# Kernel optimization log

Measured on AMD Instinct MI355X. Metric: run time of the kernel, lower is better.

The kernel has to match this reference:

```python
import jax, jax.numpy as jnp
import numpy as np

# Explicit-duration HSMM forward DP in log space.
# Recursion (all quantities in log space):
#   entry[t, j] = pi[j]                                   if t == 0
#               = logsumexp_i alpha[t-1, i] + A[i, j]      otherwise
#   alpha[t, j] = logsumexp_{d=1..min(Dmax, t+1)}
#                   entry[t-d+1, j] + D[j, d] + sum_{u=t-d+1..t} log_B[u, j]
#   loglik      = logsumexp_j alpha[T-1, j]

NEG = -1.0e30  # finite -inf sentinel (autodiff-safe)
B, T, S, DMAX = 64, 2048, 128, 128


def setup_inputs() -> dict:
    key = jax.random.key(0)
    k1, k2, k3, k4 = jax.random.split(key, 4)
    # emission log-likelihoods per (batch, time, state); need not normalize over states
    log_B = jax.random.normal(k1, (B, T, S), dtype=jnp.float32)
    # normalized log-prob buffers, matching the module's buffer constraints
    pi_logits = jax.nn.log_softmax(jax.random.normal(k2, (S,), dtype=jnp.float32))
    A_raw = jax.random.normal(k3, (S, S), dtype=jnp.float32)
    # SEMI transition constraint: no self-transitions (diagonal ~ -inf), rows normalized
    A_logits = jax.nn.log_softmax(
        jnp.where(jnp.eye(S, dtype=bool), -1.0e9, A_raw), axis=1)
    D_logits = jax.nn.log_softmax(
        jax.random.normal(k4, (S, DMAX), dtype=jnp.float32), axis=1)
    return {"log_B": log_B, "pi_logits": pi_logits,
            "A_logits": A_logits, "D_logits": D_logits}


def _hsmm_forward_loglik(log_B, pi_logits, A_logits, D_logits):
    Bn, Tn, Sn = log_B.shape
    Dm = D_logits.shape[1]
    lb = jnp.transpose(log_B, (1, 0, 2))                         # (T, B, S)
    # cum[k] = sum_{u < k} log_B[u]; front-padded with Dm zero rows (masked anyway)
    cum = jnp.concatenate(
        [jnp.zeros((1, Bn, Sn), lb.dtype), jnp.cumsum(lb, axis=0)], axis=0)
    cum_pad = jnp.concatenate(
        [jnp.zeros((Dm, Bn, Sn), lb.dtype), cum], axis=0)        # (T+Dm+1, B, S)
    logD = D_logits.T[:, None, :]                                # (Dm, 1, S)
    dur = jnp.arange(1, Dm + 1)[:, None, None]                   # (Dm, 1, 1)

    def step(carry, t):
        entry_buf, alpha_prev = carry                            # (Dm,B,S), (B,S)
        # transition into state j after a segment ended at t-1
        trans = jax.nn.logsumexp(
            alpha_prev[:, :, None] + A_logits[None, :, :], axis=1)  # (B, S)
        entry_t = jnp.where(t == 0, pi_logits[None, :], trans)
        # entry_buf[d-1] = entry[t-d+1]
        entry_buf = jnp.roll(entry_buf, 1, axis=0).at[0].set(entry_t)
        # segment emission sums: seg[d-1] = cum[t+1] - cum[t+1-d]
        win = jax.lax.dynamic_slice_in_dim(cum_pad, t + 1, Dm, axis=0)
        end = jax.lax.dynamic_slice_in_dim(cum_pad, t + Dm + 1, 1, axis=0)
        seg = end - jnp.flip(win, axis=0)                        # (Dm, B, S)
        scores = entry_buf + logD + seg
        scores = jnp.where(dur <= t + 1, scores, NEG)            # mask d > t+1
        alpha_t = jax.nn.logsumexp(scores, axis=0)               # (B, S)
        return (entry_buf, alpha_t), None

    init = (jnp.full((Dm, Bn, Sn), NEG, lb.dtype),
            jnp.full((Bn, Sn), NEG, lb.dtype))
    (_, alpha_last), _ = jax.lax.scan(step, init, jnp.arange(Tn))
    return jax.nn.logsumexp(alpha_last, axis=1)                  # (B,)


def reference(log_B, pi_logits, A_logits, D_logits):
    return _hsmm_forward_loglik(log_B, pi_logits, A_logits, D_logits)
```

## Files before the change

kernel.cpp:

```cpp
#include <hip/hip_runtime.h>

#define TT 2048
#define SS 128
#define DMAXX 128
#define NBATCH 64

typedef float f2 __attribute__((ext_vector_type(2)));

__device__ __forceinline__ float fexp2(float x){ return __builtin_amdgcn_exp2f(x); }
__device__ __forceinline__ float flog2(float x){ return __builtin_amdgcn_logf(x); }
__device__ __forceinline__ float frcp (float x){ return __builtin_amdgcn_rcpf(x); }
__device__ __forceinline__ f2 pkfma(f2 a, f2 b, f2 c){ return __builtin_elementwise_fma(a, b, c); }

template<int CTRL>
__device__ __forceinline__ float dppf(float x) {
    int i = __float_as_int(x);
    return __int_as_float(__builtin_amdgcn_update_dpp(i, i, CTRL, 0xF, 0xF, false));
}
template<int CTRL>
__device__ __forceinline__ float dppzf(float x) {
    int i = __float_as_int(x);
    return __int_as_float(__builtin_amdgcn_update_dpp(0, i, CTRL, 0xF, 0xF, true));
}
#define DPP_XOR1   0xB1
#define DPP_XOR2   0x4E
#define DPP_RSHR4  0x114
#define DPP_ROR4   0x124
#define DPP_ROR8   0x128
#define DPP_BC15   0x142
#define DPP_BC31   0x143

constexpr float LOG2E = 1.4426950408889634f;
constexpr float LN2   = 0.6931471805599453f;

struct State {
    f2    rp[16];
    f2    eApk[16];
    f2    eDp[32];
    float eD0;
    float pf[4];
    const float* pfp;
    float C2;
    float e_pi;
    float G;
    float dsP;
};

struct Ctx {
    const float4* up0; const float4* up1;
    const f2*     wmp;
    float* uaw0; float* uaw1;
    float* wmwp;
    bool q0, l63, b0, b1;
};

template<int P>
__device__ __forceinline__ void hsmm_step(State& st, const Ctx& c, int tb8)
{
    constexpr int  rho    = 31 - P;
    constexpr int  rhoN   = 30 - P;
    constexpr int  pb     = (P + 1) & 1;
    constexpr int  wb     = P & 1;
    constexpr bool DO_WM  = (P == 6);
    constexpr bool DO_RN  = (P == 7);
    constexpr bool REBASE = (P == 7);
    const int t = tb8 + P;

    const float4* up = pb ? c.up1 : c.up0;
    float4 va = up[0];
    float4 vb = up[1];

    float xB = st.pf[P & 3];
    if (t + 4 < TT) st.pf[P & 3] = st.pfp[P * SS];
    if constexpr (P == 7) st.pfp += 8 * SS;

    float g = fexp2(xB * LOG2E);
    if constexpr (DO_RN) {
        f2 wv = *c.wmp;
        float m = fmaxf(wv.x, wv.y);
        m = fmaxf(m, dppf<DPP_XOR1>(m));
        m = fmaxf(m, dppf<DPP_XOR2>(m));
        st.C2 += flog2(m);
        g *= frcp(m);
    }
    float rG = frcp(st.G);
    float Gn = st.G * g;
    st.G = Gn;

    f2 a0, a1, a2, a3, u;
    u = (f2){va.x, va.y};
    a0 = u * st.eApk[0];  a1 = u * st.eApk[4];  a2 = u * st.eApk[8];  a3 = u * st.eApk[12];
    u = (f2){va.z, va.w};
    a0 = pkfma(u, st.eApk[1], a0); a1 = pkfma(u, st.eApk[5], a1);
    a2 = pkfma(u, st.eApk[9], a2); a3 = pkfma(u, st.eApk[13], a3);
    u = (f2){vb.x, vb.y};
    a0 = pkfma(u, st.eApk[2], a0); a1 = pkfma(u, st.eApk[6], a1);
    a2 = pkfma(u, st.eApk[10], a2); a3 = pkfma(u, st.eApk[14], a3);
    u = (f2){vb.z, vb.w};
    a0 = pkfma(u, st.eApk[3], a0); a1 = pkfma(u, st.eApk[7], a1);
    a2 = pkfma(u, st.eApk[11], a2); a3 = pkfma(u, st.eApk[15], a3);

    float h0 = a0.x + a0.y, h1 = a1.x + a1.y, h2 = a2.x + a2.y, h3 = a3.x + a3.y;
    float s1 = c.b0 ? h0 : h1;
    float k1 = c.b0 ? h1 : h0;
    float m01 = k1 + dppf<DPP_XOR1>(s1);
    float s2 = c.b0 ? h2 : h3;
    float k2 = c.b0 ? h3 : h2;
    float m23 = k2 + dppf<DPP_XOR1>(s2);
    float s3 = c.b1 ? m01 : m23;
    float k3 = c.b1 ? m23 : m01;
    float tp = k3 + dppf<DPP_XOR2>(s3);
    tp += dppf<DPP_ROR4>(tp);
    tp += dppf<DPP_ROR8>(tp);
    if constexpr (P == 0) { if (tb8 == 0) tp = st.e_pi; }

    float U = fmaf(tp * g, st.eD0, st.dsP * Gn);
    if (c.q0) {
        float fr = tp * rG;
        if constexpr (rho & 1) st.rp[rho >> 1].y = fr;
        else                   st.rp[rho >> 1].x = fr;
        *(wb ? c.uaw1 : c.uaw0) = U;
    }

    if constexpr (DO_WM) {
        float wm = U;
        wm = fmaxf(wm, dppf<DPP_XOR1>(wm));
        wm = fmaxf(wm, dppf<DPP_XOR2>(wm));
        wm = fmaxf(wm, dppf<DPP_BC15>(wm));
        wm = fmaxf(wm, dppf<DPP_BC31>(wm));
        if (c.l63) *c.wmwp = wm;
    }

    if constexpr (REBASE) {
        f2 GG = {Gn, Gn};
#pragma unroll
        for (int m2 = 0; m2 < 16; ++m2) st.rp[m2] = st.rp[m2] * GG;
        st.G = 1.f;
    }

    float rold;
    if constexpr (rhoN & 1) rold = st.rp[rhoN >> 1].y; else rold = st.rp[rhoN >> 1].x;
    float ins = dppzf<DPP_RSHR4>(rold);
    if constexpr (rhoN & 1) st.rp[rhoN >> 1].y = ins;
    else                    st.rp[rhoN >> 1].x = ins;

    f2 q0a = {0.f, 0.f}, q1a = {0.f, 0.f}, q2a = {0.f, 0.f}, q3a = {0.f, 0.f};
#pragma unroll
    for (int m2 = 0; m2 < 16; m2 += 4) {
        q0a = pkfma(st.rp[m2],     st.eDp[(2 * m2 + P + 2) & 31], q0a);
        q1a = pkfma(st.rp[m2 + 1], st.eDp[(2 * m2 + P + 4) & 31], q1a);
        q2a = pkfma(st.rp[m2 + 2], st.eDp[(2 * m2 + P + 6) & 31], q2a);
        q3a = pkfma(st.rp[m2 + 3], st.eDp[(2 * m2 + P + 8) & 31], q3a);
    }
    f2 qs = (q0a + q1a) + (q2a + q3a);
    float ds = qs.x + qs.y;
    ds += dppf<DPP_ROR4>(ds);
    ds += dppf<DPP_ROR8>(ds);
    st.dsP = ds;

    asm volatile("s_waitcnt lgkmcnt(0)\n\ts_barrier" ::: "memory");
}

__launch_bounds__(512, 2)
__global__ void hsmm_fwd_kernel(const float* __restrict__ logB,
                                const float* __restrict__ pi,
                                const float* __restrict__ A,
                                const float* __restrict__ D,
                                float* __restrict__ out)
{
    const int b    = blockIdx.x;
    const int tid  = threadIdx.x;
    const int l    = tid & 63;
    const int w    = tid >> 6;
    const int r    = (l >> 4);
    const int sIdx = l & 15;
    const int cc   = l & 3;
    const int q    = (l >> 2) & 3;
    const int j4   = w * 16 + r * 4;
    const int j    = j4 + cc;

    __shared__ __align__(16) float ua[2][16 * 12];
    __shared__ __align__(16) float wmaxf[8];

    State st;
#pragma unroll
    for (int cp = 0; cp < 4; ++cp)
#pragma unroll
        for (int m = 0; m < 4; ++m) {
            st.eApk[cp * 4 + m].x = fexp2(A[(8 * sIdx + 2 * m)     * SS + j4 + cp] * LOG2E);
            st.eApk[cp * 4 + m].y = fexp2(A[(8 * sIdx + 2 * m + 1) * SS + j4 + cp] * LOG2E);
        }
    {
        float eD[32];
#pragma unroll
        for (int k = 0; k < 32; ++k)
            eD[k] = fexp2(D[j * DMAXX + q * 32 + k] * LOG2E);
#pragma unroll
        for (int wdx = 0; wdx < 32; ++wdx) {
            st.eDp[wdx].x = eD[wdx];
            st.eDp[wdx].y = eD[(wdx + 1) & 31];
        }
    }
#pragma unroll
    for (int k = 0; k < 16; ++k) st.rp[k] = (f2){0.f, 0.f};
    st.eD0  = fexp2(D[j * DMAXX] * LOG2E);
    st.C2   = 0.f;
    st.e_pi = fexp2(pi[j] * LOG2E);
    st.G    = 1.f;
    st.dsP  = 0.f;

    const float* __restrict__ lb = logB + ((size_t)b * TT) * SS + j;
#pragma unroll
    for (int k = 0; k < 4; ++k) st.pf[k] = lb[(size_t)k * SS];
    st.pfp = lb + (size_t)4 * SS;

    Ctx c;
    c.up0  = (const float4*)&ua[0][sIdx * 12];
    c.up1  = (const float4*)&ua[1][sIdx * 12];
    c.wmp  = (const f2*)&wmaxf[2 * cc];
    c.q0   = (q == 0);
    c.l63  = (l == 63);
    c.b0   = (l & 1);
    c.b1   = ((l & 2) != 0);
    c.uaw0 = &ua[0][(j >> 3) * 12 + (j & 7)];
    c.uaw1 = &ua[1][(j >> 3) * 12 + (j & 7)];
    c.wmwp = &wmaxf[w];

#pragma unroll 1
    for (int tb8 = 0; tb8 < TT; tb8 += 8) {
        hsmm_step<0>(st, c, tb8); hsmm_step<1>(st, c, tb8);
        hsmm_step<2>(st, c, tb8); hsmm_step<3>(st, c, tb8);
        hsmm_step<4>(st, c, tb8); hsmm_step<5>(st, c, tb8);
        hsmm_step<6>(st, c, tb8); hsmm_step<7>(st, c, tb8);
        {
            f2 t12 = st.rp[12], t13 = st.rp[13], t14 = st.rp[14], t15 = st.rp[15];
            st.rp[15] = st.rp[11]; st.rp[14] = st.rp[10];
            st.rp[13] = st.rp[9];  st.rp[12] = st.rp[8];
            st.rp[11] = st.rp[7];  st.rp[10] = st.rp[6];
            st.rp[9]  = st.rp[5];  st.rp[8]  = st.rp[4];
            st.rp[7]  = st.rp[3];  st.rp[6]  = st.rp[2];
            st.rp[5]  = st.rp[1];  st.rp[4]  = st.rp[0];
            st.rp[3] = t15; st.rp[2] = t14; st.rp[1] = t13; st.rp[0] = t12;
        }
    }

    if (tid == 0) {
        float s = 0.f;
        for (int i = 0; i < SS; ++i) s += ua[1][(i >> 3) * 12 + (i & 7)];
        out[b] = (st.C2 + flog2(s)) * LN2;
    }
}

extern "C" void kernel_launch(void* const* d_in, const int* in_sizes, int n_in,
                              void* d_out, int out_size, void* d_ws, size_t ws_size,
                              hipStream_t stream) {
    const float* logB = (const float*)d_in[0];
    const float* pi   = (const float*)d_in[1];
    const float* A    = (const float*)d_in[2];
    const float* D    = (const float*)d_in[3];
    float* out        = (float*)d_out;
    hipLaunchKernelGGL(hsmm_fwd_kernel, dim3(NBATCH), dim3(512), 0, stream,
                       logB, pi, A, D, out);
}
```

Measured before the change: 825.6 us.

## Halve block to 256 threads with each lane owning two states

The block shrinks from 8 waves to 4, and each thread now carries two state roles (j and j+64), each with its own A, D and ring registers. The per-step barrier then synchronises fewer waves, the max reduction spans 4 waves instead of 8, and the shared transition input read is reused for both roles. In exchange, per-thread register pressure roughly doubles and each wave's serial dependency chain gets longer, which risks spills and longer per-step latency.

```diff
diff --git a/kernel.cpp b/kernel.cpp
--- a/kernel.cpp
+++ b/kernel.cpp
@@ -33,14 +33,12 @@
 constexpr float LOG2E = 1.4426950408889634f;
 constexpr float LN2   = 0.6931471805599453f;
 
-struct State {
+struct Role {
     f2    rp[16];
     f2    eApk[16];
     f2    eDp[32];
     float eD0;
     float pf[4];
-    const float* pfp;
-    float C2;
     float e_pi;
     float G;
     float dsP;
@@ -48,82 +46,132 @@
 
 struct Ctx {
     const float4* up0; const float4* up1;
-    const f2*     wmp;
-    float* uaw0; float* uaw1;
+    const float*  wmp;
+    float* uawA0; float* uawA1;
+    float* uawB0; float* uawB1;
     float* wmwp;
     bool q0, l63, b0, b1;
 };
 
+__device__ __forceinline__ float trans_reduce(float4 va, float4 vb,
+                                              const f2* eApk, bool b0, bool b1)
+{
+    f2 a0, a1, a2, a3, u;
+    u = (f2){va.x, va.y};
+    a0 = u * eApk[0];  a1 = u * eApk[4];  a2 = u * eApk[8];  a3 = u * eApk[12];
+    u = (f2){va.z, va.w};
+    a0 = pkfma(u, eApk[1], a0); a1 = pkfma(u, eApk[5], a1);
+    a2 = pkfma(u, eApk[9], a2); a3 = pkfma(u, eApk[13], a3);
+    u = (f2){vb.x, vb.y};
+    a0 = pkfma(u, eApk[2], a0); a1 = pkfma(u, eApk[6], a1);
+    a2 = pkfma(u, eApk[10], a2); a3 = pkfma(u, eApk[14], a3);
+    u = (f2){vb.z, vb.w};
+    a0 = pkfma(u, eApk[3], a0); a1 = pkfma(u, eApk[7], a1);
+    a2 = pkfma(u, eApk[11], a2); a3 = pkfma(u, eApk[15], a3);
+    float h0 = a0.x + a0.y, h1 = a1.x + a1.y, h2 = a2.x + a2.y, h3 = a3.x + a3.y;
+    float s1 = b0 ? h0 : h1;
+    float k1 = b0 ? h1 : h0;
+    float m01 = k1 + dppf<DPP_XOR1>(s1);
+    float s2 = b0 ? h2 : h3;
+    float k2 = b0 ? h3 : h2;
+    float m23 = k2 + dppf<DPP_XOR1>(s2);
+    float s3 = b1 ? m01 : m23;
+    float k3 = b1 ? m23 : m01;
+    float tp = k3 + dppf<DPP_XOR2>(s3);
+    tp += dppf<DPP_ROR4>(tp);
+    tp += dppf<DPP_ROR8>(tp);
+    return tp;
+}
+
 template<int P>
-__device__ __forceinline__ void hsmm_step(State& st, const Ctx& c, int tb8)
-{
-    constexpr int  rho    = 31 - P;
-    constexpr int  rhoN   = 30 - P;
-    constexpr int  pb     = (P + 1) & 1;
-    constexpr int  wb     = P & 1;
-    constexpr bool DO_WM  = (P == 6);
-    constexpr bool DO_RN  = (P == 7);
-    constexpr bool REBASE = (P == 7);
+__device__ __forceinline__ void tail_dur(Role& R)
+{
+    constexpr int rhoN = 30 - P;
+    float rold;
+    if constexpr (rhoN & 1) rold = R.rp[rhoN >> 1].y; else rold = R.rp[rhoN >> 1].x;
+    float ins = dppzf<DPP_RSHR4>(rold);
+    if constexpr (rhoN & 1) R.rp[rhoN >> 1].y = ins;
+    else                    R.rp[rhoN >> 1].x = ins;
+
+    f2 q0a = {0.f, 0.f}, q1a = {0.f, 0.f}, q2a = {0.f, 0.f}, q3a = {0.f, 0.f};
+#pragma unroll
+    for (int m2 = 0; m2 < 16; m2 += 4) {
+        q0a = pkfma(R.rp[m2],     R.eDp[(2 * m2 + P + 2) & 31], q0a);
+        q1a = pkfma(R.rp[m2 + 1], R.eDp[(2 * m2 + P + 4) & 31], q1a);
+        q2a = pkfma(R.rp[m2 + 2], R.eDp[(2 * m2 + P + 6) & 31], q2a);
+        q3a = pkfma(R.rp[m2 + 3], R.eDp[(2 * m2 + P + 8) & 31], q3a);
+    }
+    f2 qs = (q0a + q1a) + (q2a + q3a);
+    float ds = qs.x + qs.y;
+    ds += dppf<DPP_ROR4>(ds);
+    ds += dppf<DPP_ROR8>(ds);
+    R.dsP = ds;
+}
+
+__device__ __forceinline__ void rotate_ring(Role& R)
+{
+    f2 t12 = R.rp[12], t13 = R.rp[13], t14 = R.rp[14], t15 = R.rp[15];
+    R.rp[15] = R.rp[11]; R.rp[14] = R.rp[10];
+    R.rp[13] = R.rp[9];  R.rp[12] = R.rp[8];
+    R.rp[11] = R.rp[7];  R.rp[10] = R.rp[6];
+    R.rp[9]  = R.rp[5];  R.rp[8]  = R.rp[4];
+    R.rp[7]  = R.rp[3];  R.rp[6]  = R.rp[2];
+    R.rp[5]  = R.rp[1];  R.rp[4]  = R.rp[0];
+    R.rp[3] = t15; R.rp[2] = t14; R.rp[1] = t13; R.rp[0] = t12;
+}
+
+template<int P>
+__device__ __forceinline__ void hsmm_step(Role& RA, Role& RB, const Ctx& c,
+                                          const float*& pfp, float& C2, int tb8)
+{
+    constexpr int  rho = 31 - P;
+    constexpr int  pb  = (P + 1) & 1;
+    constexpr int  wb  = P & 1;
     const int t = tb8 + P;
 
     const float4* up = pb ? c.up1 : c.up0;
     float4 va = up[0];
     float4 vb = up[1];
 
-    float xB = st.pf[P & 3];
-    if (t + 4 < TT) st.pf[P & 3] = st.pfp[P * SS];
-    if constexpr (P == 7) st.pfp += 8 * SS;
-
-    float g = fexp2(xB * LOG2E);
-    if constexpr (DO_RN) {
-        f2 wv = *c.wmp;
-        float m = fmaxf(wv.x, wv.y);
-        m = fmaxf(m, dppf<DPP_XOR1>(m));
-        m = fmaxf(m, dppf<DPP_XOR2>(m));
-        st.C2 += flog2(m);
-        g *= frcp(m);
-    }
-    float rG = frcp(st.G);
-    float Gn = st.G * g;
-    st.G = Gn;
-
-    f2 a0, a1, a2, a3, u;
-    u = (f2){va.x, va.y};
-    a0 = u * st.eApk[0];  a1 = u * st.eApk[4];  a2 = u * st.eApk[8];  a3 = u * st.eApk[12];
-    u = (f2){va.z, va.w};
-    a0 = pkfma(u, st.eApk[1], a0); a1 = pkfma(u, st.eApk[5], a1);
-    a2 = pkfma(u, st.eApk[9], a2); a3 = pkfma(u, st.eApk[13], a3);
-    u = (f2){vb.x, vb.y};
-    a0 = pkfma(u, st.eApk[2], a0); a1 = pkfma(u, st.eApk[6], a1);
-    a2 = pkfma(u, st.eApk[10], a2); a3 = pkfma(u, st.eApk[14], a3);
-    u = (f2){vb.z, vb.w};
-    a0 = pkfma(u, st.eApk[3], a0); a1 = pkfma(u, st.eApk[7], a1);
-    a2 = pkfma(u, st.eApk[11], a2); a3 = pkfma(u, st.eApk[15], a3);
-
-    float h0 = a0.x + a0.y, h1 = a1.x + a1.y, h2 = a2.x + a2.y, h3 = a3.x + a3.y;
-    float s1 = c.b0 ? h0 : h1;
-    float k1 = c.b0 ? h1 : h0;
-    float m01 = k1 + dppf<DPP_XOR1>(s1);
-    float s2 = c.b0 ? h2 : h3;
-    float k2 = c.b0 ? h3 : h2;
-    float m23 = k2 + dppf<DPP_XOR1>(s2);
-    float s3 = c.b1 ? m01 : m23;
-    float k3 = c.b1 ? m23 : m01;
-    float tp = k3 + dppf<DPP_XOR2>(s3);
-    tp += dppf<DPP_ROR4>(tp);
-    tp += dppf<DPP_ROR8>(tp);
-    if constexpr (P == 0) { if (tb8 == 0) tp = st.e_pi; }
-
-    float U = fmaf(tp * g, st.eD0, st.dsP * Gn);
+    float xA = RA.pf[P & 3];
+    float xB = RB.pf[P & 3];
+    if (t + 4 < TT) {
+        RA.pf[P & 3] = pfp[P * SS];
+        RB.pf[P & 3] = pfp[P * SS + 64];
+    }
+
+    float gA = fexp2(xA * LOG2E);
+    float gB = fexp2(xB * LOG2E);
+    if constexpr (P == 7) {
+        float mv = *c.wmp;
+        mv = fmaxf(mv, dppf<DPP_XOR1>(mv));
+        mv = fmaxf(mv, dppf<DPP_XOR2>(mv));
+        C2 += flog2(mv);
+        float rm = frcp(mv);
+        gA *= rm; gB *= rm;
+        pfp += 8 * SS;
+    }
+    float rGA = frcp(RA.G), rGB = frcp(RB.G);
+    float GnA = RA.G * gA;  RA.G = GnA;
+    float GnB = RB.G * gB;  RB.G = GnB;
+
+    float tpA = trans_reduce(va, vb, RA.eApk, c.b0, c.b1);
+    float tpB = trans_reduce(va, vb, RB.eApk, c.b0, c.b1);
+    if constexpr (P == 0) { if (tb8 == 0) { tpA = RA.e_pi; tpB = RB.e_pi; } }
+
+    float UA = fmaf(tpA * gA, RA.eD0, RA.dsP * GnA);
+    float UB = fmaf(tpB * gB, RB.eD0, RB.dsP * GnB);
     if (c.q0) {
-        float fr = tp * rG;
-        if constexpr (rho & 1) st.rp[rho >> 1].y = fr;
-        else                   st.rp[rho >> 1].x = fr;
-        *(wb ? c.uaw1 : c.uaw0) = U;
-    }
-
-    if constexpr (DO_WM) {
-        float wm = U;
+        float frA = tpA * rGA;
+        float frB = tpB * rGB;
+        if constexpr (rho & 1) { RA.rp[rho >> 1].y = frA; RB.rp[rho >> 1].y = frB; }
+        else                   { RA.rp[rho >> 1].x = frA; RB.rp[rho >> 1].x = frB; }
+        *(wb ? c.uawA1 : c.uawA0) = UA;
+        *(wb ? c.uawB1 : c.uawB0) = UB;
+    }
+
+    if constexpr (P == 6) {
+        float wm = fmaxf(UA, UB);
         wm = fmaxf(wm, dppf<DPP_XOR1>(wm));
         wm = fmaxf(wm, dppf<DPP_XOR2>(wm));
         wm = fmaxf(wm, dppf<DPP_BC15>(wm));
@@ -131,123 +179,119 @@
         if (c.l63) *c.wmwp = wm;
     }
 
-    if constexpr (REBASE) {
-        f2 GG = {Gn, Gn};
-#pragma unroll
-        for (int m2 = 0; m2 < 16; ++m2) st.rp[m2] = st.rp[m2] * GG;
-        st.G = 1.f;
-    }
-
-    float rold;
-    if constexpr (rhoN & 1) rold = st.rp[rhoN >> 1].y; else rold = st.rp[rhoN >> 1].x;
-    float ins = dppzf<DPP_RSHR4>(rold);
-    if constexpr (rhoN & 1) st.rp[rhoN >> 1].y = ins;
-    else                    st.rp[rhoN >> 1].x = ins;
-
-    f2 q0a = {0.f, 0.f}, q1a = {0.f, 0.f}, q2a = {0.f, 0.f}, q3a = {0.f, 0.f};
-#pragma unroll
-    for (int m2 = 0; m2 < 16; m2 += 4) {
-        q0a = pkfma(st.rp[m2],     st.eDp[(2 * m2 + P + 2) & 31], q0a);
-        q1a = pkfma(st.rp[m2 + 1], st.eDp[(2 * m2 + P + 4) & 31], q1a);
-        q2a = pkfma(st.rp[m2 + 2], st.eDp[(2 * m2 + P + 6) & 31], q2a);
-        q3a = pkfma(st.rp[m2 + 3], st.eDp[(2 * m2 + P + 8) & 31], q3a);
-    }
-    f2 qs = (q0a + q1a) + (q2a + q3a);
-    float ds = qs.x + qs.y;
-    ds += dppf<DPP_ROR4>(ds);
-    ds += dppf<DPP_ROR8>(ds);
-    st.dsP = ds;
+    if constexpr (P == 7) {
+        f2 GGA = {GnA, GnA}, GGB = {GnB, GnB};
+#pragma unroll
+        for (int m2 = 0; m2 < 16; ++m2) {
+            RA.rp[m2] = RA.rp[m2] * GGA;
+            RB.rp[m2] = RB.rp[m2] * GGB;
+        }
+        RA.G = 1.f; RB.G = 1.f;
+    }
+
+    tail_dur<P>(RA);
+    tail_dur<P>(RB);
 
     asm volatile("s_waitcnt lgkmcnt(0)\n\ts_barrier" ::: "memory");
 }
 
-__launch_bounds__(512, 2)
+__launch_bounds__(256, 1)
 __global__ void hsmm_fwd_kernel(const float* __restrict__ logB,
                                 const float* __restrict__ pi,
-                                const float* __restrict__ A,
-                                const float* __restrict__ D,
+                                const float* __restrict__ Ag,
+                                const float* __restrict__ Dg,
                                 float* __restrict__ out)
 {
     const int b    = blockIdx.x;
     const int tid  = threadIdx.x;
     const int l    = tid & 63;
-    const int w    = tid >> 6;
+    const int wv   = tid >> 6;
     const int r    = (l >> 4);
     const int sIdx = l & 15;
     const int cc   = l & 3;
     const int q    = (l >> 2) & 3;
-    const int j4   = w * 16 + r * 4;
-    const int j    = j4 + cc;
+    const int j4A  = wv * 16 + r * 4;
+    const int jA   = j4A + cc;
+    const int jB   = jA + 64;
 
     __shared__ __align__(16) float ua[2][16 * 12];
-    __shared__ __align__(16) float wmaxf[8];
-
-    State st;
+    __shared__ __align__(16) float wmaxf[4];
+
+    Role RA, RB;
 #pragma unroll
     for (int cp = 0; cp < 4; ++cp)
 #pragma unroll
         for (int m = 0; m < 4; ++m) {
-            st.eApk[cp * 4 + m].x = fexp2(A[(8 * sIdx + 2 * m)     * SS + j4 + cp] * LOG2E);
-            st.eApk[cp * 4 + m].y = fexp2(A[(8 * sIdx + 2 * m + 1) * SS + j4 + cp] * LOG2E);
+            RA.eApk[cp * 4 + m].x = fexp2(Ag[(8 * sIdx + 2 * m)     * SS + j4A + cp] * LOG2E);
+            RA.eApk[cp * 4 + m].y = fexp2(Ag[(8 * sIdx + 2 * m + 1) * SS + j4A + cp] * LOG2E);
+            RB.eApk[cp * 4 + m].x = fexp2(Ag[(8 * sIdx + 2 * m)     * SS + j4A + 64 + cp] * LOG2E);
+            RB.eApk[cp * 4 + m].y = fexp2(Ag[(8 * sIdx + 2 * m + 1) * SS + j4A + 64 + cp] * LOG2E);
         }
     {
-        float eD[32];
-#pragma unroll
-        for (int k = 0; k < 32; ++k)
-            eD[k] = fexp2(D[j * DMAXX + q * 32 + k] * LOG2E);
+        float eDA[32], eDB[32];
+#pragma unroll
+        for (int k = 0; k < 32; ++k) {
+            eDA[k] = fexp2(Dg[jA * DMAXX + q * 32 + k] * LOG2E);
+            eDB[k] = fexp2(Dg[jB * DMAXX + q * 32 + k] * LOG2E);
+        }
 #pragma unroll
         for (int wdx = 0; wdx < 32; ++wdx) {
-            st.eDp[wdx].x = eD[wdx];
-            st.eDp[wdx].y = eD[(wdx + 1) & 31];
+            RA.eDp[wdx].x = eDA[wdx];
+            RA.eDp[wdx].y = eDA[(wdx + 1) & 31];
+            RB.eDp[wdx].x = eDB[wdx];
+            RB.eDp[wdx].y = eDB[(wdx + 1) & 31];
         }
     }
 #pragma unroll
-    for (int k = 0; k < 16; ++k) st.rp[k] = (f2){0.f, 0.f};
-    st.eD0  = fexp2(D[j * DMAXX] * LOG2E);
-    st.C2   = 0.f;
-    st.e_pi = fexp2(pi[j] * LOG2E);
-    st.G    = 1.f;
-    st.dsP  = 0.f;
-
-    const float* __restrict__ lb = logB + ((size_t)b * TT) * SS + j;
-#pragma unroll
-    for (int k = 0; k < 4; ++k) st.pf[k] = lb[(size_t)k * SS];
-    st.pfp = lb + (size_t)4 * SS;
+    for (int k = 0; k < 16; ++k) { RA.rp[k] = (f2){0.f, 0.f}; RB.rp[k] = (f2){0.f, 0.f}; }
+    RA.eD0  = fexp2(Dg[jA * DMAXX] * LOG2E);
+    RB.eD0  = fexp2(Dg[jB * DMAXX] * LOG2E);
+    RA.e_pi = fexp2(pi[jA] * LOG2E);
+    RB.e_pi = fexp2(pi[jB] * LOG2E);
+    RA.G = 1.f; RB.G = 1.f;
+    RA.dsP = 0.f; RB.dsP = 0.f;
+    float C2 = 0.f;
+
+    const float* __restrict__ lb = logB + ((size_t)b * TT) * SS + jA;
+#pragma unroll
+    for (int k = 0; k < 4; ++k) {
+        RA.pf[k] = lb[(size_t)k * SS];
+        RB.pf[k] = lb[(size_t)k * SS + 64];
+    }
+    const float* pfp = lb + (size_t)4 * SS;
 
     Ctx c;
-    c.up0  = (const float4*)&ua[0][sIdx * 12];
-    c.up1  = (const float4*)&ua[1][sIdx * 12];
-    c.wmp  = (const f2*)&wmaxf[2 * cc];
-    c.q0   = (q == 0);
-    c.l63  = (l == 63);
-    c.b0   = (l & 1);
-    c.b1   = ((l & 2) != 0);
-    c.uaw0 = &ua[0][(j >> 3) * 12 + (j & 7)];
-    c.uaw1 = &ua[1][(j >> 3) * 12 + (j & 7)];
-    c.wmwp = &wmaxf[w];
+    c.up0   = (const float4*)&ua[0][sIdx * 12];
+    c.up1   = (const float4*)&ua[1][sIdx * 12];
+    c.wmp   = &wmaxf[cc];
+    c.q0    = (q == 0);
+    c.l63   = (l == 63);
+    c.b0    = (l & 1);
+    c.b1    = ((l & 2) != 0);
+    c.uawA0 = &ua[0][(jA >> 3) * 12 + (jA & 7)];
+    c.uawA1 = &ua[1][(jA >> 3) * 12 + (jA & 7)];
+    c.uawB0 = &ua[0][(jB >> 3) * 12 + (jB & 7)];
+    c.uawB1 = &ua[1][(jB >> 3) * 12 + (jB & 7)];
+    c.wmwp  = &wmaxf[wv];
 
 #pragma unroll 1
     for (int tb8 = 0; tb8 < TT; tb8 += 8) {
-        hsmm_step<0>(st, c, tb8); hsmm_step<1>(st, c, tb8);
-        hsmm_step<2>(st, c, tb8); hsmm_step<3>(st, c, tb8);
-        hsmm_step<4>(st, c, tb8); hsmm_step<5>(st, c, tb8);
-        hsmm_step<6>(st, c, tb8); hsmm_step<7>(st, c, tb8);
-        {
-            f2 t12 = st.rp[12], t13 = st.rp[13], t14 = st.rp[14], t15 = st.rp[15];
-            st.rp[15] = st.rp[11]; st.rp[14] = st.rp[10];
-            st.rp[13] = st.rp[9];  st.rp[12] = st.rp[8];
-            st.rp[11] = st.rp[7];  st.rp[10] = st.rp[6];
-            st.rp[9]  = st.rp[5];  st.rp[8]  = st.rp[4];
-            st.rp[7]  = st.rp[3];  st.rp[6]  = st.rp[2];
-            st.rp[5]  = st.rp[1];  st.rp[4]  = st.rp[0];
-            st.rp[3] = t15; st.rp[2] = t14; st.rp[1] = t13; st.rp[0] = t12;
-        }
+        hsmm_step<0>(RA, RB, c, pfp, C2, tb8);
+        hsmm_step<1>(RA, RB, c, pfp, C2, tb8);
+        hsmm_step<2>(RA, RB, c, pfp, C2, tb8);
+        hsmm_step<3>(RA, RB, c, pfp, C2, tb8);
+        hsmm_step<4>(RA, RB, c, pfp, C2, tb8);
+        hsmm_step<5>(RA, RB, c, pfp, C2, tb8);
+        hsmm_step<6>(RA, RB, c, pfp, C2, tb8);
+        hsmm_step<7>(RA, RB, c, pfp, C2, tb8);
+        rotate_ring(RA);
+        rotate_ring(RB);
     }
 
     if (tid == 0) {
         float s = 0.f;
         for (int i = 0; i < SS; ++i) s += ua[1][(i >> 3) * 12 + (i & 7)];
-        out[b] = (st.C2 + flog2(s)) * LN2;
+        out[b] = (C2 + flog2(s)) * LN2;
     }
 }
 
@@ -259,6 +303,6 @@
     const float* A    = (const float*)d_in[2];
     const float* D    = (const float*)d_in[3];
     float* out        = (float*)d_out;
-    hipLaunchKernelGGL(hsmm_fwd_kernel, dim3(NBATCH), dim3(512), 0, stream,
+    hipLaunchKernelGGL(hsmm_fwd_kernel, dim3(NBATCH), dim3(256), 0, stream,
                        logB, pi, A, D, out);
 }
```

Measured after the change: 1.031 ms. +24.8%, slower.

## Split transition sum by source-state quarter and unroll time loop to 16

Applied to the files above, without the earlier changes.

Each lane now holds the exp-transition weights for its own destination state over one quarter of the source states. The partial sums are combined with the same row rotations already used for the duration reduction, which removes the XOR-DPP butterfly and per-lane select logic. In exchange each lane does more LDS float4 reads per step. The time loop is also unrolled to 16 steps, so the register ring-buffer rotation is a swap of halves done half as often, with renormalisation still every 8 steps.

```diff
diff --git a/kernel.cpp b/kernel.cpp
--- a/kernel.cpp
+++ b/kernel.cpp
@@ -51,28 +51,51 @@
     const f2*     wmp;
     float* uaw0; float* uaw1;
     float* wmwp;
-    bool q0, l63, b0, b1;
+    bool q0, l63;
 };
 
+__device__ __forceinline__ float trans_reduce(const float4* up, const f2* eApk)
+{
+    float4 v0 = up[0], v1 = up[1], v2 = up[3], v3 = up[4],
+           v4 = up[6], v5 = up[7], v6 = up[9], v7 = up[10];
+    f2 a0, a1, a2, a3, u;
+    u = (f2){v0.x, v0.y}; a0 = u * eApk[0];
+    u = (f2){v0.z, v0.w}; a1 = u * eApk[1];
+    u = (f2){v1.x, v1.y}; a2 = u * eApk[2];
+    u = (f2){v1.z, v1.w}; a3 = u * eApk[3];
+    u = (f2){v2.x, v2.y}; a0 = pkfma(u, eApk[4],  a0);
+    u = (f2){v2.z, v2.w}; a1 = pkfma(u, eApk[5],  a1);
+    u = (f2){v3.x, v3.y}; a2 = pkfma(u, eApk[6],  a2);
+    u = (f2){v3.z, v3.w}; a3 = pkfma(u, eApk[7],  a3);
+    u = (f2){v4.x, v4.y}; a0 = pkfma(u, eApk[8],  a0);
+    u = (f2){v4.z, v4.w}; a1 = pkfma(u, eApk[9],  a1);
+    u = (f2){v5.x, v5.y}; a2 = pkfma(u, eApk[10], a2);
+    u = (f2){v5.z, v5.w}; a3 = pkfma(u, eApk[11], a3);
+    u = (f2){v6.x, v6.y}; a0 = pkfma(u, eApk[12], a0);
+    u = (f2){v6.z, v6.w}; a1 = pkfma(u, eApk[13], a1);
+    u = (f2){v7.x, v7.y}; a2 = pkfma(u, eApk[14], a2);
+    u = (f2){v7.z, v7.w}; a3 = pkfma(u, eApk[15], a3);
+    f2 qs = (a0 + a1) + (a2 + a3);
+    float tp = qs.x + qs.y;
+    tp += dppf<DPP_ROR4>(tp);
+    tp += dppf<DPP_ROR8>(tp);
+    return tp;
+}
+
 template<int P>
-__device__ __forceinline__ void hsmm_step(State& st, const Ctx& c, int tb8)
+__device__ __forceinline__ void hsmm_step(State& st, const Ctx& c, int tb16)
 {
     constexpr int  rho    = 31 - P;
     constexpr int  rhoN   = 30 - P;
     constexpr int  pb     = (P + 1) & 1;
     constexpr int  wb     = P & 1;
-    constexpr bool DO_WM  = (P == 6);
-    constexpr bool DO_RN  = (P == 7);
-    constexpr bool REBASE = (P == 7);
-    const int t = tb8 + P;
-
-    const float4* up = pb ? c.up1 : c.up0;
-    float4 va = up[0];
-    float4 vb = up[1];
+    constexpr bool DO_WM  = ((P & 7) == 6);
+    constexpr bool DO_RN  = ((P & 7) == 7);
+    const int t = tb16 + P;
 
     float xB = st.pf[P & 3];
-    if (t + 4 < TT) st.pf[P & 3] = st.pfp[P * SS];
-    if constexpr (P == 7) st.pfp += 8 * SS;
+    if (t + 4 < TT) st.pf[P & 3] = st.pfp[(P & 7) * SS];
+    if constexpr (DO_RN) st.pfp += 8 * SS;
 
     float g = fexp2(xB * LOG2E);
     if constexpr (DO_RN) {
@@ -87,32 +110,8 @@
     float Gn = st.G * g;
     st.G = Gn;
 
-    f2 a0, a1, a2, a3, u;
-    u = (f2){va.x, va.y};
-    a0 = u * st.eApk[0];  a1 = u * st.eApk[4];  a2 = u * st.eApk[8];  a3 = u * st.eApk[12];
-    u = (f2){va.z, va.w};
-    a0 = pkfma(u, st.eApk[1], a0); a1 = pkfma(u, st.eApk[5], a1);
-    a2 = pkfma(u, st.eApk[9], a2); a3 = pkfma(u, st.eApk[13], a3);
-    u = (f2){vb.x, vb.y};
-    a0 = pkfma(u, st.eApk[2], a0); a1 = pkfma(u, st.eApk[6], a1);
-    a2 = pkfma(u, st.eApk[10], a2); a3 = pkfma(u, st.eApk[14], a3);
-    u = (f2){vb.z, vb.w};
-    a0 = pkfma(u, st.eApk[3], a0); a1 = pkfma(u, st.eApk[7], a1);
-    a2 = pkfma(u, st.eApk[11], a2); a3 = pkfma(u, st.eApk[15], a3);
-
-    float h0 = a0.x + a0.y, h1 = a1.x + a1.y, h2 = a2.x + a2.y, h3 = a3.x + a3.y;
-    float s1 = c.b0 ? h0 : h1;
-    float k1 = c.b0 ? h1 : h0;
-    float m01 = k1 + dppf<DPP_XOR1>(s1);
-    float s2 = c.b0 ? h2 : h3;
-    float k2 = c.b0 ? h3 : h2;
-    float m23 = k2 + dppf<DPP_XOR1>(s2);
-    float s3 = c.b1 ? m01 : m23;
-    float k3 = c.b1 ? m23 : m01;
-    float tp = k3 + dppf<DPP_XOR2>(s3);
-    tp += dppf<DPP_ROR4>(tp);
-    tp += dppf<DPP_ROR8>(tp);
-    if constexpr (P == 0) { if (tb8 == 0) tp = st.e_pi; }
+    float tp = trans_reduce(pb ? c.up1 : c.up0, st.eApk);
+    if constexpr (P == 0) { if (tb16 == 0) tp = st.e_pi; }
 
     float U = fmaf(tp * g, st.eD0, st.dsP * Gn);
     if (c.q0) {
@@ -131,7 +130,7 @@
         if (c.l63) *c.wmwp = wm;
     }
 
-    if constexpr (REBASE) {
+    if constexpr (DO_RN) {
         f2 GG = {Gn, Gn};
 #pragma unroll
         for (int m2 = 0; m2 < 16; ++m2) st.rp[m2] = st.rp[m2] * GG;
@@ -184,12 +183,10 @@
 
     State st;
 #pragma unroll
-    for (int cp = 0; cp < 4; ++cp)
-#pragma unroll
-        for (int m = 0; m < 4; ++m) {
-            st.eApk[cp * 4 + m].x = fexp2(A[(8 * sIdx + 2 * m)     * SS + j4 + cp] * LOG2E);
-            st.eApk[cp * 4 + m].y = fexp2(A[(8 * sIdx + 2 * m + 1) * SS + j4 + cp] * LOG2E);
-        }
+    for (int k = 0; k < 16; ++k) {
+        st.eApk[k].x = fexp2(A[(32 * q + 2 * k)     * SS + j] * LOG2E);
+        st.eApk[k].y = fexp2(A[(32 * q + 2 * k + 1) * SS + j] * LOG2E);
+    }
     {
         float eD[32];
 #pragma unroll
@@ -215,32 +212,30 @@
     st.pfp = lb + (size_t)4 * SS;
 
     Ctx c;
-    c.up0  = (const float4*)&ua[0][sIdx * 12];
-    c.up1  = (const float4*)&ua[1][sIdx * 12];
+    c.up0  = (const float4*)&ua[0][48 * q];
+    c.up1  = (const float4*)&ua[1][48 * q];
     c.wmp  = (const f2*)&wmaxf[2 * cc];
     c.q0   = (q == 0);
     c.l63  = (l == 63);
-    c.b0   = (l & 1);
-    c.b1   = ((l & 2) != 0);
     c.uaw0 = &ua[0][(j >> 3) * 12 + (j & 7)];
     c.uaw1 = &ua[1][(j >> 3) * 12 + (j & 7)];
     c.wmwp = &wmaxf[w];
 
 #pragma unroll 1
-    for (int tb8 = 0; tb8 < TT; tb8 += 8) {
-        hsmm_step<0>(st, c, tb8); hsmm_step<1>(st, c, tb8);
-        hsmm_step<2>(st, c, tb8); hsmm_step<3>(st, c, tb8);
-        hsmm_step<4>(st, c, tb8); hsmm_step<5>(st, c, tb8);
-        hsmm_step<6>(st, c, tb8); hsmm_step<7>(st, c, tb8);
-        {
-            f2 t12 = st.rp[12], t13 = st.rp[13], t14 = st.rp[14], t15 = st.rp[15];
-            st.rp[15] = st.rp[11]; st.rp[14] = st.rp[10];
-            st.rp[13] = st.rp[9];  st.rp[12] = st.rp[8];
-            st.rp[11] = st.rp[7];  st.rp[10] = st.rp[6];
-            st.rp[9]  = st.rp[5];  st.rp[8]  = st.rp[4];
-            st.rp[7]  = st.rp[3];  st.rp[6]  = st.rp[2];
-            st.rp[5]  = st.rp[1];  st.rp[4]  = st.rp[0];
-            st.rp[3] = t15; st.rp[2] = t14; st.rp[1] = t13; st.rp[0] = t12;
+    for (int tb16 = 0; tb16 < TT; tb16 += 16) {
+        hsmm_step< 0>(st, c, tb16); hsmm_step< 1>(st, c, tb16);
+        hsmm_step< 2>(st, c, tb16); hsmm_step< 3>(st, c, tb16);
+        hsmm_step< 4>(st, c, tb16); hsmm_step< 5>(st, c, tb16);
+        hsmm_step< 6>(st, c, tb16); hsmm_step< 7>(st, c, tb16);
+        hsmm_step< 8>(st, c, tb16); hsmm_step< 9>(st, c, tb16);
+        hsmm_step<10>(st, c, tb16); hsmm_step<11>(st, c, tb16);
+        hsmm_step<12>(st, c, tb16); hsmm_step<13>(st, c, tb16);
+        hsmm_step<14>(st, c, tb16); hsmm_step<15>(st, c, tb16);
+#pragma unroll
+        for (int i = 0; i < 8; ++i) {
+            f2 tmp = st.rp[i];
+            st.rp[i] = st.rp[i + 8];
+            st.rp[i + 8] = tmp;
         }
     }
 
```

Result: no change. 837.6 us (+1.4%).
